# Optimization experiments

Hardware: AMD Instinct MI355X
Metric: run time of the kernel (lower is better)

The kernel has to match this reference:

```python
import jax, jax.numpy as jnp
import numpy as np

G, NPG = 2048, 512          # glimpses, points per glimpse
N0 = G * NPG                # 1,048,576 input points
CPG, CPG2 = 128, 32         # clusters per glimpse at level1/level2
M1, M2 = G * CPG, G * CPG2  # 262144, 65536


def _seg_mean_np(x, ids, m):
    cnt = np.bincount(ids, minlength=m).astype(np.float32)
    out = np.stack([np.bincount(ids, weights=x[:, d], minlength=m) for d in range(x.shape[1])], axis=1)
    return (out / np.maximum(cnt, 1.0)[:, None]).astype(np.float32)


def setup_inputs() -> dict:
    key = jax.random.key(0)
    ks = jax.random.split(key, 16)
    rng = np.random.default_rng(0)
    pos_np = (rng.random((N0, 3)) * 4.0).astype(np.float32)
    # voxel_mean_pool level 0: each point -> a cluster within its glimpse
    g_of_pt = np.arange(N0) // NPG
    out_index0 = (g_of_pt * CPG + rng.integers(0, CPG, N0)).astype(np.int64)
    pos1_np = _seg_mean_np(pos_np, out_index0, M1)
    g_of_c1 = np.arange(M1) // CPG
    out_index1 = (g_of_c1 * CPG2 + rng.integers(0, CPG2, M1)).astype(np.int64)
    pos2_np = _seg_mean_np(pos1_np, out_index1, M2)
    out_index2 = (np.arange(M2) // CPG2).astype(np.int64)  # glimpse id per level-2 point

    def w(k, shp, s=0.05):
        return jax.random.normal(k, shp, dtype=jnp.float32) * s

    return {
        "rgb": jax.random.normal(ks[0], (N0, 1), dtype=jnp.float32),
        "pos": jnp.asarray(pos_np), "pos1": jnp.asarray(pos1_np), "pos2": jnp.asarray(pos2_np),
        "out_index0": jnp.asarray(out_index0), "out_index1": jnp.asarray(out_index1),
        "out_index2": jnp.asarray(out_index2),
        "eps": jax.random.normal(ks[1], (G, 128), dtype=jnp.float32),
        # conv1: local (c_in=1 + 3 -> 16), global (16 -> 32)
        "W1l": w(ks[2], (4, 16)), "b1l": jnp.zeros(16), "W1g": w(ks[3], (16, 32)), "b1g": jnp.zeros(32),
        # conv2: (32+3 -> 64), (64 -> 128)
        "W2l": w(ks[4], (35, 64)), "b2l": jnp.zeros(64), "W2g": w(ks[5], (64, 128)), "b2g": jnp.zeros(128),
        # conv3: (128+3 -> 128), (128 -> 256)
        "W3l": w(ks[6], (131, 128)), "b3l": jnp.zeros(128), "W3g": w(ks[7], (128, 256)), "b3g": jnp.zeros(256),
        "Wlin": w(ks[8], (256, 256)), "blin": jnp.zeros(256),
    }


def _point_conv(x_in, pos_in, pos_out, out_index, Wl, bl, Wg, bg):
    # gather relative position of each input point w.r.t. its output center
    rel = pos_in - pos_out[out_index]                      # [E,3]
    h = jax.nn.celu(jnp.concatenate([x_in, rel], -1) @ Wl + bl)  # per-edge MLP
    m = pos_out.shape[0]
    cnt = jax.ops.segment_sum(jnp.ones((h.shape[0],), h.dtype), out_index, num_segments=m)
    agg = jax.ops.segment_sum(h, out_index, num_segments=m) / jnp.maximum(cnt, 1.0)[:, None]
    return agg @ Wg + bg


def reference(rgb, pos, pos1, pos2, out_index0, out_index1, out_index2, eps,
              W1l, b1l, W1g, b1g, W2l, b2l, W2g, b2g, W3l, b3l, W3g, b3g, Wlin, blin):
    f = rgb  # ar=False path: feature = rgb
    f = jax.nn.celu(_point_conv(f, pos, pos1, out_index0, W1l, b1l, W1g, b1g))   # [M1,32]
    f = jax.nn.celu(_point_conv(f, pos1, pos2, out_index1, W2l, b2l, W2g, b2g))  # [M2,128]
    centers = jnp.zeros((G, 3), f.dtype)  # pos_sample = zeros_like(glimpse__center)
    f = jax.nn.celu(_point_conv(f, pos2, centers, out_index2, W3l, b3l, W3g, b3g))  # [G,256]
    out = f @ Wlin + blin
    mu, sg = jnp.split(out, 2, axis=1)
    sigma = jax.nn.softplus(sg)  # to_sigma
    z = mu + sigma * eps         # Normal.rsample
    z_what, z_mask = jnp.split(z, 2, axis=1)
    return z_what, z_mask, mu, sigma, f
```

## Files before the change

kernel.cpp:

```cpp
#include <hip/hip_runtime.h>
#include <hip/hip_bf16.h>
#include <cstddef>

#define G_   2048
#define NPG_ 512
#define CPG_ 128
#define CPG2_ 32

#define OFF_ZW 0
#define OFF_ZM (G_*64)
#define OFF_MU (2*G_*64)
#define OFF_SG (2*G_*64 + G_*128)
#define OFF_F  (2*G_*64 + 2*G_*128)

typedef __attribute__((ext_vector_type(8))) short bf16x8;
typedef __attribute__((ext_vector_type(4))) float f32x4;
typedef _Float16 f16x2 __attribute__((ext_vector_type(2)));

__device__ __forceinline__ float celu_f(float x)     { return x > 0.f ? x : __expf(x) - 1.f; }
__device__ __forceinline__ float softplus_f(float x) { return fmaxf(x, 0.f) + __logf(1.f + __expf(-fabsf(x))); }
__device__ __forceinline__ unsigned short f2bf(float x) {
    unsigned u = __float_as_uint(x);
    u += 0x7FFFu + ((u >> 16) & 1u);
    return (unsigned short)(u >> 16);
}
__device__ __forceinline__ unsigned pack2(float a, float b) {
    unsigned ua = __float_as_uint(a); ua += 0x7FFFu + ((ua >> 16) & 1u);
    unsigned ub = __float_as_uint(b); ub += 0x7FFFu + ((ub >> 16) & 1u);
    return (ua >> 16) | (ub & 0xFFFF0000u);
}
__device__ __forceinline__ bf16x8 ldb8(const unsigned short* p) {
    union { uint2 u[2]; bf16x8 v; } x;
    x.u[0] = *(const uint2*)p;
    x.u[1] = *(const uint2*)(p + 4);
    return x.v;
}

__global__ void k_prep(const float* __restrict__ W2l, const float* __restrict__ W2g,
                       const float* __restrict__ W3l, const float* __restrict__ W3g,
                       const float* __restrict__ Wlin, const float* __restrict__ W1g,
                       unsigned short* __restrict__ w2lT, unsigned short* __restrict__ w2gT,
                       unsigned short* __restrict__ w3lT, unsigned short* __restrict__ w3gT,
                       unsigned short* __restrict__ wlinT, unsigned short* __restrict__ w1gT)
{
    const int tid = blockIdx.x*256 + threadIdx.x, stride = gridDim.x*256;
    for (int i = tid; i < 64*64; i += stride) {
        const int ch = i >> 6, k = i & 63;
        w2lT[i] = f2bf(k < 35 ? W2l[k*64 + ch] : 0.f);
    }
    for (int i = tid; i < 128*64; i += stride) {
        const int ch = i >> 6, k = i & 63;
        w2gT[i] = f2bf(W2g[k*128 + ch]);
    }
    for (int i = tid; i < 128*160; i += stride) {
        const int ch = i / 160, k = i % 160;
        w3lT[i] = f2bf(k < 131 ? W3l[k*128 + ch] : 0.f);
    }
    for (int i = tid; i < 256*128; i += stride) {
        const int ch = i >> 7, k = i & 127;
        w3gT[i] = f2bf(W3g[k*256 + ch]);
    }
    for (int i = tid; i < 256*256; i += stride) {
        const int ch = i >> 8, k = i & 255;
        wlinT[i] = f2bf(Wlin[k*256 + ch]);
    }
    for (int i = tid; i < 32*40; i += stride) {
        const int ch = i / 40, k = i % 40;
        w1gT[i] = f2bf(k < 16 ? W1g[k*32 + ch] : 0.f);
    }
}

__global__ __launch_bounds__(256, 6) void k_fused(
    const float* __restrict__ rgb, const float* __restrict__ pos, const float* __restrict__ pos1,
    const float* __restrict__ pos2, const int* __restrict__ idx0, const int* __restrict__ idx1,
    const float* __restrict__ W1l, const float* __restrict__ b1l,
    const unsigned short* __restrict__ w1gT, const float* __restrict__ b1g,
    const unsigned short* __restrict__ w2lT, const float* __restrict__ b2l,
    const unsigned short* __restrict__ w2gT, const float* __restrict__ b2g,
    const unsigned short* __restrict__ w3lT, const float* __restrict__ b3l,
    unsigned short* __restrict__ aggws)
{
    const int g = blockIdx.x, t = threadIdx.x;
    const int lane = t & 63, wv = t >> 6;
    const int lr = lane & 15, quad = lane >> 4;

    __shared__ __align__(16) unsigned char smem[27008];
    unsigned short* const spts2 = (unsigned short*)smem;
    unsigned short* const aggT  = (unsigned short*)(smem + 16384);
    unsigned short* const xs16  = (unsigned short*)smem;
    unsigned short* const HT    = (unsigned short*)smem;
    unsigned short* const xs3   = (unsigned short*)smem;
    int* const cnt  = (int*)(smem + 25600);
    int* const ctr  = (int*)(smem + 26112);
    int* const cnti = (int*)(smem + 26624);
    int* const wtot = (int*)(smem + 26752);
    unsigned short* const sT   = (unsigned short*)(smem + 18432);
    unsigned short* const agg2 = (unsigned short*)(smem + 18432);
    float* const red  = (float*)(smem + 18432);
    float* const invc = (float*)(smem + 26880);

    if (t < CPG_)  cnt[t]  = 0;
    if (t < CPG2_) cnti[t] = 0;
    int slc_r = 0;
    float relx = 0.f, rely = 0.f, relz = 0.f;
    if (t < CPG_) {
        const int c2 = idx1[g*CPG_ + t];
        slc_r = c2 - g*CPG2_;
        relx = pos1[(g*CPG_ + t)*3 + 0] - pos2[c2*3 + 0];
        rely = pos1[(g*CPG_ + t)*3 + 1] - pos2[c2*3 + 1];
        relz = pos1[(g*CPG_ + t)*3 + 2] - pos2[c2*3 + 2];
    }
    for (int i = t; i < 128*8; i += 256) {
        const int r = i >> 3, j = i & 7;
        ((unsigned*)aggT)[r*18 + 8 + j] = 0u;
    }
    const bf16x8 w1g_b0 = *(const bf16x8*)&w1gT[(0*16 + lr)*40 + quad*8];
    const bf16x8 w1g_b1 = *(const bf16x8*)&w1gT[(1*16 + lr)*40 + quad*8];
    const float  b1g_0 = b1g[lr], b1g_1 = b1g[16 + lr];
    __syncthreads();

    unsigned hpk[2][8];
    int plc[2];
    {
        float px0[2], prx[2], pry[2], prz[2];
        #pragma unroll
        for (int r = 0; r < 2; r++) {
            const int lp = r*256 + t;
            const int p  = g*NPG_ + lp;
            const int c  = idx0[p];
            plc[r] = c - g*CPG_;
            px0[r] = rgb[p];
            prx[r] = pos[p*3+0] - pos1[c*3+0];
            pry[r] = pos[p*3+1] - pos1[c*3+1];
            prz[r] = pos[p*3+2] - pos1[c*3+2];
            atomicAdd(&cnt[plc[r]], 1);
        }
        if (t < CPG_) atomicAdd(&cnti[slc_r], 1);
        #pragma unroll
        for (int j = 0; j < 16; j += 2) {
            const float wj0 = W1l[j],   wx0 = W1l[16+j],   wy0 = W1l[32+j],   wz0 = W1l[48+j],   bb0 = b1l[j];
            const float wj1 = W1l[j+1], wx1 = W1l[16+j+1], wy1 = W1l[32+j+1], wz1 = W1l[48+j+1], bb1 = b1l[j+1];
            #pragma unroll
            for (int r = 0; r < 2; r++) {
                const float h0 = celu_f(bb0 + px0[r]*wj0 + prx[r]*wx0 + pry[r]*wy0 + prz[r]*wz0);
                const float h1 = celu_f(bb1 + px0[r]*wj1 + prx[r]*wx1 + pry[r]*wy1 + prz[r]*wz1);
                union { f16x2 h; unsigned u; } pk;
                pk.h[0] = (_Float16)h0;
                pk.h[1] = (_Float16)h1;
                hpk[r][j >> 1] = pk.u;
            }
        }
    }
    __syncthreads();

    if (t < CPG_) {
        int val = cnt[t];
        const int ln = t & 63;
        #pragma unroll
        for (int d = 1; d < 64; d <<= 1) {
            const int v = __shfl_up(val, d, 64);
            if (ln >= d) val += v;
        }
        ctr[t] = val - cnt[t];
        if (t == 63) *wtot = val;
    }
    __syncthreads();
    if (t >= 64 && t < CPG_) ctr[t] += *wtot;
    if (t < CPG2_) invc[t] = 1.f / fmaxf((float)cnti[t], 1.f);
    __syncthreads();

    #pragma unroll
    for (int r = 0; r < 2; r++) {
        const int slot = atomicAdd(&ctr[plc[r]], 1);
        uint4 q0, q1;
        q0.x = hpk[r][0]; q0.y = hpk[r][1]; q0.z = hpk[r][2]; q0.w = hpk[r][3];
        q1.x = hpk[r][4]; q1.y = hpk[r][5]; q1.z = hpk[r][6]; q1.w = hpk[r][7];
        *(uint4*)&spts2[slot*16]     = q0;
        *(uint4*)&spts2[slot*16 + 8] = q1;
    }
    __syncthreads();

    {
        const int c = t >> 1, half = t & 1;
        const int n = cnt[c];
        const int base = ctr[c] - n;
        const int n0 = (n + 1) >> 1;
        const int sI = base + (half ? n0 : 0);
        const int eI = base + (half ? n  : n0);
        f16x2 acc[8];
        #pragma unroll
        for (int j = 0; j < 8; j++) { union { unsigned u; f16x2 h; } z; z.u = 0u; acc[j] = z.h; }
        for (int i = sI; i < eI; i++) {
            const uint4 a = *(const uint4*)&spts2[i*16];
            const uint4 b = *(const uint4*)&spts2[i*16 + 8];
            union { unsigned u; f16x2 h; } w;
            w.u = a.x; acc[0] += w.h;  w.u = a.y; acc[1] += w.h;
            w.u = a.z; acc[2] += w.h;  w.u = a.w; acc[3] += w.h;
            w.u = b.x; acc[4] += w.h;  w.u = b.y; acc[5] += w.h;
            w.u = b.z; acc[6] += w.h;  w.u = b.w; acc[7] += w.h;
        }
        #pragma unroll
        for (int j = 0; j < 8; j++) {
            union { unsigned u; f16x2 h; } s, o;
            s.h = acc[j];
            o.u = __shfl_xor(s.u, 1);
            acc[j] += o.h;
        }
        const float inv = 1.f / fmaxf((float)n, 1.f);
        const int ch0 = half * 8, j0 = half * 4;
        float v[8];
        #pragma unroll
        for (int k = 0; k < 4; k++) {
            v[2*k]   = (float)acc[j0+k][0] * inv;
            v[2*k+1] = (float)acc[j0+k][1] * inv;
        }
        uint2 q0, q1;
        q0.x = pack2(v[0], v[1]); q0.y = pack2(v[2], v[3]);
        q1.x = pack2(v[4], v[5]); q1.y = pack2(v[6], v[7]);
        *(uint2*)&aggT[c*36 + ch0]     = q0;
        *(uint2*)&aggT[c*36 + ch0 + 4] = q1;
    }
    __syncthreads();

    f32x4 c1[2][2];
    {
        c1[0][0] = (f32x4){b1g_0, b1g_0, b1g_0, b1g_0};
        c1[0][1] = c1[0][0];
        c1[1][0] = (f32x4){b1g_1, b1g_1, b1g_1, b1g_1};
        c1[1][1] = c1[1][0];
        #pragma unroll
        for (int mt = 0; mt < 2; mt++) {
            const bf16x8 a = ldb8(&aggT[((2*wv + mt)*16 + lr)*36 + quad*8]);
            c1[0][mt] = __builtin_amdgcn_mfma_f32_16x16x32_bf16(a, w1g_b0, c1[0][mt], 0, 0, 0);
            c1[1][mt] = __builtin_amdgcn_mfma_f32_16x16x32_bf16(a, w1g_b1, c1[1][mt], 0, 0, 0);
        }
    }
    __syncthreads();

    {
        const uint4 z4 = {0u, 0u, 0u, 0u};
        for (int i = t; i < 528; i += 256) ((uint4*)sT)[i] = z4;
    }
    #pragma unroll
    for (int nt = 0; nt < 2; nt++)
    #pragma unroll
    for (int mt = 0; mt < 2; mt++)
    #pragma unroll
    for (int r = 0; r < 4; r++) {
        const int cl = (2*wv + mt)*16 + quad*4 + r;
        xs16[cl*72 + nt*16 + lr] = f2bf(celu_f(c1[nt][mt][r]));
    }
    if (t < CPG_) {
        xs16[t*72 + 32] = f2bf(relx);
        xs16[t*72 + 33] = f2bf(rely);
        xs16[t*72 + 34] = f2bf(relz);
    }
    for (int i = t; i < 128*29; i += 256) {
        const int r = i / 29, c = 35 + (i - r*29);
        xs16[r*72 + c] = 0;
    }
    __syncthreads();

    if (t < CPG_) sT[slc_r*132 + t] = 0x3F80;
    float hv[8][4];
    {
        const int chn = wv*16 + lr;
        const bf16x8 bw0 = *(const bf16x8*)&w2lT[chn*64 + quad*8];
        const bf16x8 bw1 = *(const bf16x8*)&w2lT[chn*64 + 32 + quad*8];
        const float bias = b2l[chn];
        #pragma unroll
        for (int m = 0; m < 8; m++) {
            f32x4 acc = (f32x4){bias, bias, bias, bias};
            const bf16x8 a0 = *(const bf16x8*)&xs16[(m*16 + lr)*72 + quad*8];
            const bf16x8 a1 = *(const bf16x8*)&xs16[(m*16 + lr)*72 + 32 + quad*8];
            acc = __builtin_amdgcn_mfma_f32_16x16x32_bf16(a0, bw0, acc, 0, 0, 0);
            acc = __builtin_amdgcn_mfma_f32_16x16x32_bf16(a1, bw1, acc, 0, 0, 0);
            #pragma unroll
            for (int r = 0; r < 4; r++) hv[m][r] = celu_f(acc[r]);
        }
    }
    __syncthreads();

    {
        const int chn = wv*16 + lr;
        #pragma unroll
        for (int m = 0; m < 8; m++) {
            uint2 p;
            p.x = pack2(hv[m][0], hv[m][1]);
            p.y = pack2(hv[m][2], hv[m][3]);
            *(uint2*)&HT[chn*136 + m*16 + quad*4] = p;
        }
    }
    __syncthreads();

    float aggv[2][4];
    {
        const int ch = wv*16 + lr;
        f32x4 acc[2];
        acc[0] = (f32x4){0.f, 0.f, 0.f, 0.f};
        acc[1] = (f32x4){0.f, 0.f, 0.f, 0.f};
        #pragma unroll
        for (int ks = 0; ks < 4; ks++) {
            const bf16x8 b = *(const bf16x8*)&HT[ch*136 + ks*32 + quad*8];
            #pragma unroll
            for (int mt = 0; mt < 2; mt++) {
                const bf16x8 a = ldb8(&sT[(mt*16 + lr)*132 + ks*32 + quad*8]);
                acc[mt] = __builtin_amdgcn_mfma_f32_16x16x32_bf16(a, b, acc[mt], 0, 0, 0);
            }
        }
        #pragma unroll
        for (int mt = 0; mt < 2; mt++)
        #pragma unroll
        for (int r = 0; r < 4; r++)
            aggv[mt][r] = acc[mt][r] * invc[mt*16 + quad*4 + r];
    }
    __syncthreads();

    {
        const int ch = wv*16 + lr;
        #pragma unroll
        for (int mt = 0; mt < 2; mt++)
        #pragma unroll
        for (int r = 0; r < 4; r++)
            agg2[(mt*16 + quad*4 + r)*72 + ch] = f2bf(aggv[mt][r]);
    }
    if (t < CPG2_) {
        #pragma unroll
        for (int d = 0; d < 3; d++)
            xs3[t*168 + 128 + d] = f2bf(pos2[(g*CPG2_ + t)*3 + d]);
    }
    for (int i = t; i < 32*29; i += 256) {
        const int r = i / 29, c = 131 + (i - r*29);
        xs3[r*168 + c] = 0;
    }
    __syncthreads();

    {
        f32x4 acc2[2][2];
        int   chn2[2];
        bf16x8 bw[2][2];
        #pragma unroll
        for (int nt = 0; nt < 2; nt++) {
            chn2[nt] = (wv + nt*4)*16 + lr;
            const float bias = b2g[chn2[nt]];
            #pragma unroll
            for (int mt = 0; mt < 2; mt++) acc2[nt][mt] = (f32x4){bias, bias, bias, bias};
            bw[nt][0] = *(const bf16x8*)&w2gT[chn2[nt]*64 + quad*8];
            bw[nt][1] = *(const bf16x8*)&w2gT[chn2[nt]*64 + 32 + quad*8];
        }
        #pragma unroll
        for (int ks = 0; ks < 2; ks++) {
            #pragma unroll
            for (int mt = 0; mt < 2; mt++) {
                const bf16x8 a = *(const bf16x8*)&agg2[(mt*16 + lr)*72 + ks*32 + quad*8];
                acc2[0][mt] = __builtin_amdgcn_mfma_f32_16x16x32_bf16(a, bw[0][ks], acc2[0][mt], 0, 0, 0);
                acc2[1][mt] = __builtin_amdgcn_mfma_f32_16x16x32_bf16(a, bw[1][ks], acc2[1][mt], 0, 0, 0);
            }
        }
        #pragma unroll
        for (int nt = 0; nt < 2; nt++)
        #pragma unroll
        for (int mt = 0; mt < 2; mt++)
        #pragma unroll
        for (int r = 0; r < 4; r++) {
            const int row = mt*16 + quad*4 + r;
            xs3[row*168 + chn2[nt]] = f2bf(celu_f(acc2[nt][mt][r]));
        }
    }
    __syncthreads();

    {
        f32x4 acc[2][2];
        int chn[2];
        #pragma unroll
        for (int nt = 0; nt < 2; nt++) {
            chn[nt] = (wv + nt*4)*16 + lr;
            const float bias = b3l[chn[nt]];
            #pragma unroll
            for (int mt = 0; mt < 2; mt++) acc[nt][mt] = (f32x4){bias, bias, bias, bias};
        }
        #pragma unroll
        for (int ks = 0; ks < 5; ks++) {
            const bf16x8 b0 = *(const bf16x8*)&w3lT[chn[0]*160 + ks*32 + quad*8];
            const bf16x8 b1 = *(const bf16x8*)&w3lT[chn[1]*160 + ks*32 + quad*8];
            #pragma unroll
            for (int mt = 0; mt < 2; mt++) {
                const bf16x8 a = *(const bf16x8*)&xs3[(mt*16 + lr)*168 + ks*32 + quad*8];
                acc[0][mt] = __builtin_amdgcn_mfma_f32_16x16x32_bf16(a, b0, acc[0][mt], 0, 0, 0);
                acc[1][mt] = __builtin_amdgcn_mfma_f32_16x16x32_bf16(a, b1, acc[1][mt], 0, 0, 0);
            }
        }
        #pragma unroll
        for (int nt = 0; nt < 2; nt++)
        #pragma unroll
        for (int mt = 0; mt < 2; mt++) {
            const float p = celu_f(acc[nt][mt][0]) + celu_f(acc[nt][mt][1])
                          + celu_f(acc[nt][mt][2]) + celu_f(acc[nt][mt][3]);
            red[chn[nt]*9 + mt*4 + quad] = p;
        }
    }
    __syncthreads();

    if (t < 128) {
        const float* rp = &red[t*9];
        float a = 0.f;
        #pragma unroll
        for (int p = 0; p < 8; p++) a += rp[p];
        aggws[(size_t)g*128 + t] = f2bf(a * (1.f/32.f));
    }
}

__global__ __launch_bounds__(256) void k_head(
    const unsigned short* __restrict__ aggws,
    const unsigned short* __restrict__ w3gT, const float* __restrict__ b3g,
    const unsigned short* __restrict__ wlinT, const float* __restrict__ blin,
    const float* __restrict__ eps, float* __restrict__ out)
{
    const int g0 = blockIdx.x * 16, t = threadIdx.x;
    const int lane = t & 63, wv = t >> 6;
    const int lr = lane & 15, quad = lane >> 4;
    __shared__ __align__(16) unsigned short aggB[16*136];
    __shared__ __align__(16) unsigned short f3B[16*264];

    {
        const int row = t >> 4, col8 = (t & 15) * 8;
        const uint4 v = ((const uint4*)aggws)[(size_t)g0*16 + t];
        *(uint4*)&aggB[row*136 + col8] = v;
    }
    __syncthreads();

    {
        f32x4 c3[4];
        int ch3[4];
        #pragma unroll
        for (int nt = 0; nt < 4; nt++) {
            ch3[nt] = (wv + nt*4)*16 + lr;
            const float bias = b3g[ch3[nt]];
            c3[nt] = (f32x4){bias, bias, bias, bias};
        }
        #pragma unroll
        for (int ks = 0; ks < 4; ks++) {
            const bf16x8 a = *(const bf16x8*)&aggB[lr*136 + ks*32 + quad*8];
            #pragma unroll
            for (int nt = 0; nt < 4; nt++) {
                const bf16x8 b = *(const bf16x8*)&w3gT[ch3[nt]*128 + ks*32 + quad*8];
                c3[nt] = __builtin_amdgcn_mfma_f32_16x16x32_bf16(a, b, c3[nt], 0, 0, 0);
            }
        }
        #pragma unroll
        for (int nt = 0; nt < 4; nt++)
        #pragma unroll
        for (int r = 0; r < 4; r++) {
            const int row = quad*4 + r;
            const float v = celu_f(c3[nt][r]);
            out[OFF_F + (size_t)(g0 + row)*256 + ch3[nt]] = v;
            f3B[row*264 + ch3[nt]] = f2bf(v);
        }
    }
    __syncthreads();

    {
        f32x4 cl[4];
        int ch4[4];
        #pragma unroll
        for (int nt = 0; nt < 4; nt++) {
            ch4[nt] = (wv + nt*4)*16 + lr;
            const float bias = blin[ch4[nt]];
            cl[nt] = (f32x4){bias, bias, bias, bias};
        }
        #pragma unroll
        for (int ks = 0; ks < 8; ks++) {
            const bf16x8 a = *(const bf16x8*)&f3B[lr*264 + ks*32 + quad*8];
            #pragma unroll
            for (int nt = 0; nt < 4; nt++) {
                const bf16x8 b = *(const bf16x8*)&wlinT[ch4[nt]*256 + ks*32 + quad*8];
                cl[nt] = __builtin_amdgcn_mfma_f32_16x16x32_bf16(a, b, cl[nt], 0, 0, 0);
            }
        }
        #pragma unroll
        for (int nt = 0; nt < 2; nt++)
        #pragma unroll
        for (int r = 0; r < 4; r++) {
            const int row = quad*4 + r;
            const int g = g0 + row;
            const int ch = ch4[nt];
            const float mu    = cl[nt][r];
            const float sigma = softplus_f(cl[nt + 2][r]);
            const float z     = mu + sigma * eps[(size_t)g*128 + ch];
            out[OFF_MU + (size_t)g*128 + ch] = mu;
            out[OFF_SG + (size_t)g*128 + ch] = sigma;
            if (nt == 0) out[OFF_ZW + (size_t)g*64 + ch] = z;
            else         out[OFF_ZM + (size_t)g*64 + (ch - 64)] = z;
        }
    }
}

extern "C" void kernel_launch(void* const* d_in, const int* in_sizes, int n_in,
                              void* d_out, int out_size, void* d_ws, size_t ws_size,
                              hipStream_t stream)
{
    const float* rgb  = (const float*)d_in[0];
    const float* pos  = (const float*)d_in[1];
    const float* pos1 = (const float*)d_in[2];
    const float* pos2 = (const float*)d_in[3];
    const int*   idx0 = (const int*)d_in[4];
    const int*   idx1 = (const int*)d_in[5];
    const float* eps  = (const float*)d_in[7];
    const float* W1l = (const float*)d_in[8],  *b1l = (const float*)d_in[9];
    const float* W1g = (const float*)d_in[10], *b1g = (const float*)d_in[11];
    const float* W2l = (const float*)d_in[12], *b2l = (const float*)d_in[13];
    const float* W2g = (const float*)d_in[14], *b2g = (const float*)d_in[15];
    const float* W3l = (const float*)d_in[16], *b3l = (const float*)d_in[17];
    const float* W3g = (const float*)d_in[18], *b3g = (const float*)d_in[19];
    const float* Wlin = (const float*)d_in[20], *blin = (const float*)d_in[21];

    unsigned short* w2lT  = (unsigned short*)d_ws;
    unsigned short* w2gT  = w2lT + 64*64;
    unsigned short* w3lT  = w2gT + 128*64;
    unsigned short* w3gT  = w3lT + 128*160;
    unsigned short* wlinT = w3gT + 256*128;
    unsigned short* w1gT  = wlinT + 256*256;
    unsigned short* aggws = w1gT + 32*40;
    float* outp = (float*)d_out;

    k_prep <<<64,    256, 0, stream>>>(W2l, W2g, W3l, W3g, Wlin, W1g,
                                       w2lT, w2gT, w3lT, w3gT, wlinT, w1gT);
    k_fused<<<G_,    256, 0, stream>>>(rgb, pos, pos1, pos2, idx0, idx1,
                                       W1l, b1l, w1gT, b1g,
                                       w2lT, b2l, w2gT, b2g, w3lT, b3l, aggws);
    k_head <<<G_/16, 256, 0, stream>>>(aggws, w3gT, b3g, wlinT, blin, eps, outp);
}
```

Measured before the change: 168.5 us.

## Store level-0 edge features as planar LDS arrays and defer per-edge MLP

Per-point packed f16 features now go into LDS as 8 planes of 512 words, replacing 32-byte interleaved rows. This is meant to reduce bank conflicts on the scattered slot writes and the segmented reads. The per-edge MLP and celu now run after the prefix scan rather than before it, and the w1g/b1g weight loads move to after the scatter. Both moves shorten live ranges and lower register pressure. The cost is eight scalar LDS accesses per edge where there were two 128-bit accesses.

```diff
diff --git a/kernel.cpp b/kernel.cpp
--- a/kernel.cpp
+++ b/kernel.cpp
@@ -85,7 +85,7 @@
     const int lr = lane & 15, quad = lane >> 4;
 
     __shared__ __align__(16) unsigned char smem[27008];
-    unsigned short* const spts2 = (unsigned short*)smem;
+    unsigned* const hplanes = (unsigned*)smem;
     unsigned short* const aggT  = (unsigned short*)(smem + 16384);
     unsigned short* const xs16  = (unsigned short*)smem;
     unsigned short* const HT    = (unsigned short*)smem;
@@ -114,43 +114,23 @@
         const int r = i >> 3, j = i & 7;
         ((unsigned*)aggT)[r*18 + 8 + j] = 0u;
     }
-    const bf16x8 w1g_b0 = *(const bf16x8*)&w1gT[(0*16 + lr)*40 + quad*8];
-    const bf16x8 w1g_b1 = *(const bf16x8*)&w1gT[(1*16 + lr)*40 + quad*8];
-    const float  b1g_0 = b1g[lr], b1g_1 = b1g[16 + lr];
-    __syncthreads();
-
-    unsigned hpk[2][8];
+    __syncthreads();
+
+    float px0[2], prx[2], pry[2], prz[2];
     int plc[2];
-    {
-        float px0[2], prx[2], pry[2], prz[2];
-        #pragma unroll
-        for (int r = 0; r < 2; r++) {
-            const int lp = r*256 + t;
-            const int p  = g*NPG_ + lp;
-            const int c  = idx0[p];
-            plc[r] = c - g*CPG_;
-            px0[r] = rgb[p];
-            prx[r] = pos[p*3+0] - pos1[c*3+0];
-            pry[r] = pos[p*3+1] - pos1[c*3+1];
-            prz[r] = pos[p*3+2] - pos1[c*3+2];
-            atomicAdd(&cnt[plc[r]], 1);
-        }
-        if (t < CPG_) atomicAdd(&cnti[slc_r], 1);
-        #pragma unroll
-        for (int j = 0; j < 16; j += 2) {
-            const float wj0 = W1l[j],   wx0 = W1l[16+j],   wy0 = W1l[32+j],   wz0 = W1l[48+j],   bb0 = b1l[j];
-            const float wj1 = W1l[j+1], wx1 = W1l[16+j+1], wy1 = W1l[32+j+1], wz1 = W1l[48+j+1], bb1 = b1l[j+1];
-            #pragma unroll
-            for (int r = 0; r < 2; r++) {
-                const float h0 = celu_f(bb0 + px0[r]*wj0 + prx[r]*wx0 + pry[r]*wy0 + prz[r]*wz0);
-                const float h1 = celu_f(bb1 + px0[r]*wj1 + prx[r]*wx1 + pry[r]*wy1 + prz[r]*wz1);
-                union { f16x2 h; unsigned u; } pk;
-                pk.h[0] = (_Float16)h0;
-                pk.h[1] = (_Float16)h1;
-                hpk[r][j >> 1] = pk.u;
-            }
-        }
-    }
+    #pragma unroll
+    for (int r = 0; r < 2; r++) {
+        const int lp = r*256 + t;
+        const int p  = g*NPG_ + lp;
+        const int c  = idx0[p];
+        plc[r] = c - g*CPG_;
+        px0[r] = rgb[p];
+        prx[r] = pos[p*3+0] - pos1[c*3+0];
+        pry[r] = pos[p*3+1] - pos1[c*3+1];
+        prz[r] = pos[p*3+2] - pos1[c*3+2];
+        atomicAdd(&cnt[plc[r]], 1);
+    }
+    if (t < CPG_) atomicAdd(&cnti[slc_r], 1);
     __syncthreads();
 
     if (t < CPG_) {
@@ -171,14 +151,27 @@
 
     #pragma unroll
     for (int r = 0; r < 2; r++) {
+        unsigned hpk[8];
+        #pragma unroll
+        for (int j = 0; j < 16; j += 2) {
+            const float h0 = celu_f(b1l[j]   + px0[r]*W1l[j]   + prx[r]*W1l[16+j]
+                                              + pry[r]*W1l[32+j]   + prz[r]*W1l[48+j]);
+            const float h1 = celu_f(b1l[j+1] + px0[r]*W1l[j+1] + prx[r]*W1l[16+j+1]
+                                              + pry[r]*W1l[32+j+1] + prz[r]*W1l[48+j+1]);
+            union { f16x2 h; unsigned u; } pk;
+            pk.h[0] = (_Float16)h0;
+            pk.h[1] = (_Float16)h1;
+            hpk[j >> 1] = pk.u;
+        }
         const int slot = atomicAdd(&ctr[plc[r]], 1);
-        uint4 q0, q1;
-        q0.x = hpk[r][0]; q0.y = hpk[r][1]; q0.z = hpk[r][2]; q0.w = hpk[r][3];
-        q1.x = hpk[r][4]; q1.y = hpk[r][5]; q1.z = hpk[r][6]; q1.w = hpk[r][7];
-        *(uint4*)&spts2[slot*16]     = q0;
-        *(uint4*)&spts2[slot*16 + 8] = q1;
-    }
-    __syncthreads();
+        #pragma unroll
+        for (int j = 0; j < 8; j++) hplanes[j*512 + slot] = hpk[j];
+    }
+    __syncthreads();
+
+    const bf16x8 w1g_b0 = *(const bf16x8*)&w1gT[lr*40 + quad*8];
+    const bf16x8 w1g_b1 = *(const bf16x8*)&w1gT[(16 + lr)*40 + quad*8];
+    const float  b1g_0 = b1g[lr], b1g_1 = b1g[16 + lr];
 
     {
         const int c = t >> 1, half = t & 1;
@@ -191,13 +184,12 @@
         #pragma unroll
         for (int j = 0; j < 8; j++) { union { unsigned u; f16x2 h; } z; z.u = 0u; acc[j] = z.h; }
         for (int i = sI; i < eI; i++) {
-            const uint4 a = *(const uint4*)&spts2[i*16];
-            const uint4 b = *(const uint4*)&spts2[i*16 + 8];
-            union { unsigned u; f16x2 h; } w;
-            w.u = a.x; acc[0] += w.h;  w.u = a.y; acc[1] += w.h;
-            w.u = a.z; acc[2] += w.h;  w.u = a.w; acc[3] += w.h;
-            w.u = b.x; acc[4] += w.h;  w.u = b.y; acc[5] += w.h;
-            w.u = b.z; acc[6] += w.h;  w.u = b.w; acc[7] += w.h;
+            #pragma unroll
+            for (int j = 0; j < 8; j++) {
+                union { unsigned u; f16x2 h; } w;
+                w.u = hplanes[j*512 + i];
+                acc[j] += w.h;
+            }
         }
         #pragma unroll
         for (int j = 0; j < 8; j++) {
```

Measured after the change: 156.6 us. 1.08x faster.
